# Kernel optimization log

Measured on AMD Instinct MI355X. Metric: run time of the kernel, lower is better.

Reference implementation:

```python
import jax, jax.numpy as jnp
import numpy as np

NINP = 850
NHID = 850
T = 128
B = 256
INITRANGE = 0.04
# DARTS published recurrent cell genotype
GENO_RECURRENT = [("sigmoid", 0), ("relu", 1), ("relu", 1), ("identity", 1),
                  ("tanh", 2), ("sigmoid", 5), ("tanh", 3), ("relu", 5)]
GENO_CONCAT = [1, 2, 3, 4, 5, 6, 7, 8]

ACT = {
    "tanh": jnp.tanh,
    "relu": jax.nn.relu,
    "sigmoid": jax.nn.sigmoid,
    "identity": lambda x: x,
}


def setup_inputs() -> dict:
    key = jax.random.key(0)
    ks = jax.random.split(key, 8)
    u = lambda k, s: jax.random.uniform(k, s, jnp.float32, -INITRANGE, INITRANGE)
    return {
        "inputs": jax.random.normal(ks[0], (T, B, NINP), jnp.float32),
        "hidden": jnp.zeros((1, B, NHID), jnp.float32),
        "W0_U": u(ks[1], (2 * NHID, 2 * NHID)),
        "W0_sigma": u(ks[2], (2 * NHID,)),
        "W0_V": u(ks[3], (2 * NHID, 2 * NHID)),
        "Ws_U": u(ks[4], (8, NHID, NHID)),
        "Ws_sigma": u(ks[5], (8, NHID)),
        "Ws_V": u(ks[6], (8, 2 * NHID, 2 * NHID)),
    }


def _lowrank_square(x, U, sig, V):
    # row == col: W = U @ diag(sig) @ V
    return ((x @ U) * sig) @ V


def _lowrank_wide(x, U, sig, V):
    # row < col (row=NHID, col=2*NHID): rectangular diag embeds rank=row into col dims
    t = (x @ U) * sig                               # [B, NHID]
    t = jnp.pad(t, ((0, 0), (0, V.shape[0] - t.shape[-1])))  # [B, 2*NHID]
    return t @ V                                    # [B, 2*NHID]


def _cell(x, h_prev, W0_U, W0_sigma, W0_V, Ws_U, Ws_sigma, Ws_V):
    xh = jnp.concatenate([x, h_prev], axis=-1)      # [B, 2*NHID]
    ch0 = _lowrank_square(xh, W0_U, W0_sigma, W0_V)  # [B, 2*NHID]
    c0 = jax.nn.sigmoid(ch0[:, :NHID])
    h0 = jnp.tanh(ch0[:, NHID:])
    s0 = h_prev + c0 * (h0 - h_prev)
    states = [s0]
    for i, (name, pred) in enumerate(GENO_RECURRENT):
        sp = states[pred]
        ch = _lowrank_wide(sp, Ws_U[i], Ws_sigma[i], Ws_V[i])
        c = jax.nn.sigmoid(ch[:, :NHID])
        hh = ACT[name](ch[:, NHID:])
        states.append(sp + c * (hh - sp))
    return jnp.mean(jnp.stack([states[i] for i in GENO_CONCAT], axis=-1), axis=-1)


def reference(inputs, hidden, W0_U, W0_sigma, W0_V, Ws_U, Ws_sigma, Ws_V):
    def step(h, x):
        h_new = _cell(x, h, W0_U, W0_sigma, W0_V, Ws_U, Ws_sigma, Ws_V)
        return h_new, h_new

    _, hiddens = jax.lax.scan(step, hidden[0], inputs)   # [T, B, NHID]
    return hiddens, hiddens[-1][None]
```

## Files before the change

### kernel.cpp

```cpp
#include <hip/hip_runtime.h>

typedef unsigned short u16;
typedef unsigned int u32;
typedef __attribute__((ext_vector_type(8))) short bf16x8;
typedef __attribute__((ext_vector_type(4))) float f32x4;

#define NHID 850
#define BATCH 256
#define TSTEPS 128
#define KPAD 896
#define KPAD0 1792
#define GRIDP 168

#define ACT_SIG 0
#define ACT_TANH 1
#define ACT_RELU 2
#define ACT_ID 3

__device__ __forceinline__ u16 f2bf(float f) {
  u32 u = __float_as_uint(f);
  u32 r = (u + 0x7fffu + ((u >> 16) & 1u)) >> 16;
  return (u16)r;
}
__device__ __forceinline__ float sigm(float x) { return 1.f / (1.f + __expf(-x)); }
__device__ __forceinline__ float act_apply(float x, int a) {
  if (a == ACT_SIG) return sigm(x);
  if (a == ACT_TANH) return 2.f * sigm(2.f * x) - 1.f;
  if (a == ACT_RELU) return fmaxf(x, 0.f);
  return x;
}

#define GLOAD_LDS16(gsrc, ldst)                                                     \
  __builtin_amdgcn_global_load_lds((const __attribute__((address_space(1))) void*)(gsrc), \
                                   (__attribute__((address_space(3))) void*)(ldst), 16, 0, 0)

__global__ void zero_kernel(uint4* p, u32 n) {
  u32 i = blockIdx.x * blockDim.x + threadIdx.x;
  const u32 stride = gridDim.x * blockDim.x;
  const uint4 z = {0u, 0u, 0u, 0u};
  for (; i < n; i += stride) p[i] = z;
}

__global__ void convert_kernel(const float* __restrict__ x, const float* __restrict__ h0,
                               u16* __restrict__ xb, u16* __restrict__ hb) {
  const u32 NX = (u32)TSTEPS * BATCH * NHID;
  u32 i = blockIdx.x * blockDim.x + threadIdx.x;
  if (i < NX) {
    const u32 tb = i / NHID, j = i - tb * NHID;
    xb[(size_t)tb * KPAD + j] = f2bf(x[i]);
  } else if (i < NX + (u32)BATCH * NHID) {
    const u32 k = i - NX;
    const u32 b = k / NHID, j = k - b * NHID;
    hb[(size_t)b * KPAD + j] = f2bf(h0[k]);
  }
}

__global__ __launch_bounds__(256) void prew0_kernel(const float* __restrict__ U,
                                                    const float* __restrict__ sig,
                                                    const float* __restrict__ V,
                                                    u16* __restrict__ outC,
                                                    u16* __restrict__ outH) {
  const int M = 1700, N = 1700, K = 1700;
  __shared__ float sA[64][17];
  __shared__ float sB[16][65];
  const int tid = threadIdx.x;
  const int tx = tid & 15, ty = tid >> 4;
  const int m0 = blockIdx.x * 64, n0 = blockIdx.y * 64;
  float acc[4][4] = {};
  for (int kb = 0; kb < K; kb += 16) {
#pragma unroll
    for (int i = 0; i < 4; ++i) {
      const int e = tid + i * 256;
      const int r = e >> 4, c = e & 15;
      const int mm = m0 + r, kk = kb + c;
      sA[r][c] = (mm < M && kk < K) ? U[(size_t)mm * K + kk] * sig[kk] : 0.f;
    }
#pragma unroll
    for (int i = 0; i < 4; ++i) {
      const int e = tid + i * 256;
      const int r = e >> 6, c = e & 63;
      const int kk = kb + r, nn = n0 + c;
      sB[r][c] = (kk < K && nn < N) ? V[(size_t)kk * N + nn] : 0.f;
    }
    __syncthreads();
#pragma unroll
    for (int k = 0; k < 16; ++k) {
      float a[4], b[4];
#pragma unroll
      for (int i = 0; i < 4; ++i) a[i] = sA[tx * 4 + i][k];
#pragma unroll
      for (int j = 0; j < 4; ++j) b[j] = sB[k][ty * 4 + j];
#pragma unroll
      for (int i = 0; i < 4; ++i)
#pragma unroll
        for (int j = 0; j < 4; ++j) acc[i][j] += a[i] * b[j];
    }
    __syncthreads();
  }
#pragma unroll
  for (int i = 0; i < 4; ++i) {
    const int m = m0 + tx * 4 + i;
    if (m >= M) continue;
    const int rp = (m < 850) ? m : m + 46;
#pragma unroll
    for (int j = 0; j < 4; ++j) {
      const int n = n0 + ty * 4 + j;
      if (n >= N) continue;
      if (n < 850) outC[(size_t)n * KPAD0 + rp] = f2bf(acc[i][j]);
      else outH[(size_t)(n - 850) * KPAD0 + rp] = f2bf(acc[i][j]);
    }
  }
}

__global__ __launch_bounds__(256) void prewn_kernel(const float* __restrict__ Uall,
                                                    const float* __restrict__ sigall,
                                                    const float* __restrict__ Vall,
                                                    u16* __restrict__ outBase) {
  const int M = 850, N = 1700, K = 850;
  const int ndi = blockIdx.z;
  const float* U = Uall + (size_t)ndi * 850 * 850;
  const float* sig = sigall + (size_t)ndi * 850;
  const float* V = Vall + (size_t)ndi * 1700 * 1700;
  u16* outC = outBase + (size_t)ndi * 2 * KPAD * KPAD;
  u16* outH = outC + (size_t)KPAD * KPAD;
  __shared__ float sA[64][17];
  __shared__ float sB[16][65];
  const int tid = threadIdx.x;
  const int tx = tid & 15, ty = tid >> 4;
  const int m0 = blockIdx.x * 64, n0 = blockIdx.y * 64;
  float acc[4][4] = {};
  for (int kb = 0; kb < K; kb += 16) {
#pragma unroll
    for (int i = 0; i < 4; ++i) {
      const int e = tid + i * 256;
      const int r = e >> 4, c = e & 15;
      const int mm = m0 + r, kk = kb + c;
      sA[r][c] = (mm < M && kk < K) ? U[(size_t)mm * K + kk] * sig[kk] : 0.f;
    }
#pragma unroll
    for (int i = 0; i < 4; ++i) {
      const int e = tid + i * 256;
      const int r = e >> 6, c = e & 63;
      const int kk = kb + r, nn = n0 + c;
      sB[r][c] = (kk < K && nn < N) ? V[(size_t)kk * 1700 + nn] : 0.f;
    }
    __syncthreads();
#pragma unroll
    for (int k = 0; k < 16; ++k) {
      float a[4], b[4];
#pragma unroll
      for (int i = 0; i < 4; ++i) a[i] = sA[tx * 4 + i][k];
#pragma unroll
      for (int j = 0; j < 4; ++j) b[j] = sB[k][ty * 4 + j];
#pragma unroll
      for (int i = 0; i < 4; ++i)
#pragma unroll
        for (int j = 0; j < 4; ++j) acc[i][j] += a[i] * b[j];
    }
    __syncthreads();
  }
#pragma unroll
  for (int i = 0; i < 4; ++i) {
    const int m = m0 + tx * 4 + i;
    if (m >= M) continue;
#pragma unroll
    for (int j = 0; j < 4; ++j) {
      const int n = n0 + ty * 4 + j;
      if (n >= N) continue;
      if (n < 850) outC[(size_t)n * KPAD + m] = f2bf(acc[i][j]);
      else outH[(size_t)(n - 850) * KPAD + m] = f2bf(acc[i][j]);
    }
  }
}

struct PArgs {
  const u16* xb;
  u16* hb;
  const u16* w0c; const u16* w0h;
  const u16* wnc[8]; const u16* wnh[8];
  const float* h0;
  float* out;
  float* sf[8];
  u16* sb[8];
  u32* bar;
};

__device__ __forceinline__ void grid_sync(u32* cnt, u32 target) {
  __syncthreads();
  if (threadIdx.x == 0) {
    __hip_atomic_fetch_add(cnt, 1u, __ATOMIC_RELEASE, __HIP_MEMORY_SCOPE_AGENT);
    while (__hip_atomic_load(cnt, __ATOMIC_RELAXED, __HIP_MEMORY_SCOPE_AGENT) < target)
      __builtin_amdgcn_s_sleep(8);
    __builtin_amdgcn_fence(__ATOMIC_ACQUIRE, "agent");
  }
  __syncthreads();
}

__device__ void gemm_stage(const u16* __restrict__ A, const u16* __restrict__ A2,
                           const u16* __restrict__ Bc, const u16* __restrict__ Bh,
                           const float* __restrict__ sp, float* __restrict__ outF,
                           u16* __restrict__ outB, int act, int Kt, int ktA, int bStride,
                           int m0, int n0, u16* lds) {
  const int tid = threadIdx.x;
  const int lane = tid & 63;
  const int w = tid >> 6;
  const int wm = (w & 1) * 32;
  const int wn = (w >> 1) * 32;
  f32x4 acc[2][2][2] = {};

  auto slot = [&](int buf, int s) { return lds + (size_t)(buf * 5 + s) * 4096; };
  auto stage = [&](int buf, int kt) {
    const u16* Asrc; int ktl;
    if (kt < ktA) { Asrc = A; ktl = kt; } else { Asrc = A2; ktl = kt - ktA; }
#pragma unroll
    for (int r2 = 0; r2 < 2; ++r2) {
      const int e = tid + 256 * r2;
      const int row = e >> 3;
      const int q = (e & 7) ^ (row & 7);
      GLOAD_LDS16(Asrc + (size_t)(m0 + row) * KPAD + ktl * 64 + q * 8, slot(buf, 0) + e * 8);
      GLOAD_LDS16(Bc + (size_t)(n0 + row) * bStride + kt * 64 + q * 8, slot(buf, 1) + e * 8);
      GLOAD_LDS16(Bh + (size_t)(n0 + row) * bStride + kt * 64 + q * 8, slot(buf, 2) + e * 8);
    }
  };

  stage(0, 0);
  int cur = 0;
  for (int kt = 0; kt < Kt; ++kt) {
    __syncthreads();
    if (kt + 1 < Kt) stage(cur ^ 1, kt + 1);
#pragma unroll
    for (int ks = 0; ks < 2; ++ks) {
      const int kg = lane >> 4;
      bf16x8 af[2], bc[2], bh[2];
#pragma unroll
      for (int mf = 0; mf < 2; ++mf) {
        const int row = wm + mf * 16 + (lane & 15);
        const int p = (ks * 4 + kg) ^ (row & 7);
        af[mf] = *(const bf16x8*)(slot(cur, 0) + row * 64 + p * 8);
      }
#pragma unroll
      for (int nf = 0; nf < 2; ++nf) {
        const int nr = wn + nf * 16 + (lane & 15);
        const int p = (ks * 4 + kg) ^ (nr & 7);
        bc[nf] = *(const bf16x8*)(slot(cur, 1) + nr * 64 + p * 8);
        bh[nf] = *(const bf16x8*)(slot(cur, 2) + nr * 64 + p * 8);
      }
#pragma unroll
      for (int mf = 0; mf < 2; ++mf)
#pragma unroll
        for (int nf = 0; nf < 2; ++nf) {
          acc[0][mf][nf] = __builtin_amdgcn_mfma_f32_16x16x32_bf16(af[mf], bc[nf], acc[0][mf][nf], 0, 0, 0);
          acc[1][mf][nf] = __builtin_amdgcn_mfma_f32_16x16x32_bf16(af[mf], bh[nf], acc[1][mf][nf], 0, 0, 0);
        }
    }
    cur ^= 1;
  }

  const int colb = n0 + wn + (lane & 15);
  const int rowb = m0 + wm + ((lane >> 4) << 2);
#pragma unroll
  for (int nf = 0; nf < 2; ++nf) {
    const int j = colb + nf * 16;
    if (j >= NHID) continue;
#pragma unroll
    for (int mf = 0; mf < 2; ++mf) {
      const int mb = rowb + mf * 16;
      const f32x4 ac = acc[0][mf][nf];
      const f32x4 ah = acc[1][mf][nf];
#pragma unroll
      for (int r = 0; r < 4; ++r) {
        const int m = mb + r;
        const float c = sigm(ac[r]);
        const float hv = act_apply(ah[r], act);
        const float spv = sp[m * NHID + j];
        const float s = spv + c * (hv - spv);
        outF[m * NHID + j] = s;
        outB[(size_t)m * KPAD + j] = f2bf(s);
      }
    }
  }
}

__device__ void final_tile(const PArgs& pa, int t, int m0, int n0, u16* lds) {
  const int tid = threadIdx.x;
  const int lane = tid & 63;
  const int w = tid >> 6;
  const int wm = (w & 1) * 32;
  const int wn = (w >> 1) * 32;
  const u16* A = pa.sb[5];
  const u16* Bp[4] = { pa.wnc[5], pa.wnh[5], pa.wnc[7], pa.wnh[7] };
  f32x4 acc[4][2][2] = {};

  auto slot = [&](int buf, int s) { return lds + (size_t)(buf * 5 + s) * 4096; };
  auto stage = [&](int buf, int kt) {
#pragma unroll
    for (int r2 = 0; r2 < 2; ++r2) {
      const int e = tid + 256 * r2;
      const int row = e >> 3;
      const int q = (e & 7) ^ (row & 7);
      GLOAD_LDS16(A + (size_t)(m0 + row) * KPAD + kt * 64 + q * 8, slot(buf, 0) + e * 8);
#pragma unroll
      for (int b = 0; b < 4; ++b)
        GLOAD_LDS16(Bp[b] + (size_t)(n0 + row) * KPAD + kt * 64 + q * 8, slot(buf, 1 + b) + e * 8);
    }
  };

  stage(0, 0);
  int cur = 0;
  for (int kt = 0; kt < 14; ++kt) {
    __syncthreads();
    if (kt + 1 < 14) stage(cur ^ 1, kt + 1);
#pragma unroll
    for (int ks = 0; ks < 2; ++ks) {
      const int kg = lane >> 4;
      bf16x8 af[2], bb[4][2];
#pragma unroll
      for (int mf = 0; mf < 2; ++mf) {
        const int row = wm + mf * 16 + (lane & 15);
        const int p = (ks * 4 + kg) ^ (row & 7);
        af[mf] = *(const bf16x8*)(slot(cur, 0) + row * 64 + p * 8);
      }
#pragma unroll
      for (int b = 0; b < 4; ++b)
#pragma unroll
        for (int nf = 0; nf < 2; ++nf) {
          const int nr = wn + nf * 16 + (lane & 15);
          const int p = (ks * 4 + kg) ^ (nr & 7);
          bb[b][nf] = *(const bf16x8*)(slot(cur, 1 + b) + nr * 64 + p * 8);
        }
#pragma unroll
      for (int b = 0; b < 4; ++b)
#pragma unroll
        for (int mf = 0; mf < 2; ++mf)
#pragma unroll
          for (int nf = 0; nf < 2; ++nf)
            acc[b][mf][nf] = __builtin_amdgcn_mfma_f32_16x16x32_bf16(af[mf], bb[b][nf], acc[b][mf][nf], 0, 0, 0);
    }
    cur ^= 1;
  }

  float* outH = pa.out + (size_t)t * BATCH * NHID;
  const int colb = n0 + wn + (lane & 15);
  const int rowb = m0 + wm + ((lane >> 4) << 2);
#pragma unroll
  for (int nf = 0; nf < 2; ++nf) {
    const int j = colb + nf * 16;
    if (j >= NHID) continue;
#pragma unroll
    for (int mf = 0; mf < 2; ++mf) {
      const int mb = rowb + mf * 16;
#pragma unroll
      for (int r = 0; r < 4; ++r) {
        const int m = mb + r;
        const int idx = m * NHID + j;
        const float s5v = pa.sf[5][idx];
        const float c6 = sigm(acc[0][mf][nf][r]);
        const float h6 = sigm(acc[1][mf][nf][r]);
        const float s6 = s5v + c6 * (h6 - s5v);
        const float c8 = sigm(acc[2][mf][nf][r]);
        const float h8 = fmaxf(acc[3][mf][nf][r], 0.f);
        const float s8 = s5v + c8 * (h8 - s5v);
        const float sum = pa.sf[1][idx] + pa.sf[2][idx] + pa.sf[3][idx] + pa.sf[4][idx]
                        + s5v + pa.sf[7][idx] + s6 + s8;
        const float h = sum * 0.125f;
        outH[idx] = h;
        pa.hb[(size_t)m * KPAD + j] = f2bf(h);
      }
    }
  }
}

__global__ __launch_bounds__(256) void cell_persist_kernel(PArgs pa) {
  __shared__ __align__(16) u16 lds[2 * 5 * 4096];
  const int bx = blockIdx.x;
  const u32 nb = gridDim.x;
  u32 gen = 0;

  for (int t = 0; t < TSTEPS; ++t) {
    const float* hprev = (t == 0) ? pa.h0 : (pa.out + (size_t)(t - 1) * BATCH * NHID);
    if (bx < 56) {
      const int m0 = (bx & 3) * 64, n0 = (bx >> 2) * 64;
      gemm_stage(pa.xb + (size_t)t * BATCH * KPAD, pa.hb, pa.w0c, pa.w0h,
                 hprev, pa.sf[0], pa.sb[0], ACT_TANH, 28, 14, KPAD0, m0, n0, lds);
    }
    grid_sync(pa.bar, ++gen * nb);
    if (bx < 56) {
      const int m0 = (bx & 3) * 64, n0 = (bx >> 2) * 64;
      gemm_stage(pa.sb[0], nullptr, pa.wnc[0], pa.wnh[0],
                 pa.sf[0], pa.sf[1], pa.sb[1], ACT_SIG, 14, 14, KPAD, m0, n0, lds);
    }
    grid_sync(pa.bar, ++gen * nb);
    if (bx < 168) {
      const int node = bx / 56, r = bx - node * 56;
      const int m0 = (r & 3) * 64, n0 = (r >> 2) * 64;
      const int act = (node == 2) ? ACT_ID : ACT_RELU;
      gemm_stage(pa.sb[1], nullptr, pa.wnc[1 + node], pa.wnh[1 + node],
                 pa.sf[1], pa.sf[2 + node], pa.sb[2 + node], act, 14, 14, KPAD, m0, n0, lds);
    }
    grid_sync(pa.bar, ++gen * nb);
    if (bx < 112) {
      const int g = bx / 56, r = bx - g * 56;
      const int m0 = (r & 3) * 64, n0 = (r >> 2) * 64;
      if (g == 0)
        gemm_stage(pa.sb[2], nullptr, pa.wnc[4], pa.wnh[4],
                   pa.sf[2], pa.sf[5], pa.sb[5], ACT_TANH, 14, 14, KPAD, m0, n0, lds);
      else
        gemm_stage(pa.sb[3], nullptr, pa.wnc[6], pa.wnh[6],
                   pa.sf[3], pa.sf[7], pa.sb[7], ACT_TANH, 14, 14, KPAD, m0, n0, lds);
    }
    grid_sync(pa.bar, ++gen * nb);
    if (bx < 56) {
      const int m0 = (bx & 3) * 64, n0 = (bx >> 2) * 64;
      final_tile(pa, t, m0, n0, lds);
    }
    grid_sync(pa.bar, ++gen * nb);
  }
}

extern "C" void kernel_launch(void* const* d_in, const int* in_sizes, int n_in,
                              void* d_out, int out_size, void* d_ws, size_t ws_size,
                              hipStream_t stream) {
  const float* x = (const float*)d_in[0];
  const float* h0 = (const float*)d_in[1];
  const float* W0U = (const float*)d_in[2];
  const float* W0s = (const float*)d_in[3];
  const float* W0V = (const float*)d_in[4];
  const float* WsU = (const float*)d_in[5];
  const float* Wss = (const float*)d_in[6];
  const float* WsV = (const float*)d_in[7];
  float* out = (float*)d_out;
  char* ws = (char*)d_ws;

  const size_t SZ_W0HALF = (size_t)KPAD * KPAD0 * 2;
  const size_t OFF_W0C = 0, OFF_W0H = SZ_W0HALF;
  const size_t OFF_WN = 2 * SZ_W0HALF;
  const size_t SZ_WNHALF = (size_t)KPAD * KPAD * 2;
  const size_t OFF_XB = OFF_WN + 16 * SZ_WNHALF;
  const size_t SZ_XB = (size_t)TSTEPS * BATCH * KPAD * 2;
  const size_t OFF_HB = OFF_XB + SZ_XB;
  const size_t SZ_HB = (size_t)BATCH * KPAD * 2;
  const size_t OFF_SF = OFF_HB + SZ_HB;
  const size_t SZ_SF = (size_t)BATCH * NHID * 4;
  const size_t OFF_SB = OFF_SF + 8 * SZ_SF;
  const size_t SZ_SB = (size_t)BATCH * KPAD * 2;
  const size_t OFF_BAR = OFF_SB + 8 * SZ_SB;
  const size_t TOTAL = OFF_BAR + 128;

  u16* w0c = (u16*)(ws + OFF_W0C);
  u16* w0h = (u16*)(ws + OFF_W0H);
  u16* wnBase = (u16*)(ws + OFF_WN);
  u16* xb = (u16*)(ws + OFF_XB);
  u16* hb = (u16*)(ws + OFF_HB);

  const size_t zbytes = (TOTAL <= ws_size) ? TOTAL : ws_size;
  zero_kernel<<<2048, 256, 0, stream>>>((uint4*)ws, (u32)((zbytes + 15) / 16));
  const u32 convTotal = (u32)TSTEPS * BATCH * NHID + (u32)BATCH * NHID;
  convert_kernel<<<(convTotal + 255) / 256, 256, 0, stream>>>(x, h0, xb, hb);
  prew0_kernel<<<dim3(27, 27), 256, 0, stream>>>(W0U, W0s, W0V, w0c, w0h);
  prewn_kernel<<<dim3(14, 27, 8), 256, 0, stream>>>(WsU, Wss, WsV, wnBase);

  PArgs pa;
  pa.xb = xb;
  pa.hb = hb;
  pa.w0c = w0c;
  pa.w0h = w0h;
  for (int i = 0; i < 8; ++i) {
    pa.wnc[i] = wnBase + (size_t)i * 2 * KPAD * KPAD;
    pa.wnh[i] = wnBase + (size_t)i * 2 * KPAD * KPAD + (size_t)KPAD * KPAD;
  }
  pa.h0 = h0;
  pa.out = out;
  for (int i = 0; i < 8; ++i) {
    pa.sf[i] = (float*)(ws + OFF_SF + (size_t)i * SZ_SF);
    pa.sb[i] = (u16*)(ws + OFF_SB + (size_t)i * SZ_SB);
  }
  pa.bar = (u32*)(ws + OFF_BAR);

  cell_persist_kernel<<<GRIDP, 256, 0, stream>>>(pa);

  hipMemcpyAsync(out + (size_t)TSTEPS * BATCH * NHID,
                 out + (size_t)(TSTEPS - 1) * BATCH * NHID,
                 (size_t)BATCH * NHID * sizeof(float), hipMemcpyDeviceToDevice, stream);
}
```

Measured before the change: 18.84 ms.

## Hoist input projection out of recurrence and keep weight slices resident in LDS

```diff
diff --git a/kernel.cpp b/kernel.cpp
--- a/kernel.cpp
+++ b/kernel.cpp
@@ -8,9 +8,8 @@
 #define NHID 850
 #define BATCH 256
 #define TSTEPS 128
-#define KPAD 896
-#define KPAD0 1792
-#define GRIDP 168
+#define KW 896
+#define GRIDP 243
 
 #define ACT_SIG 0
 #define ACT_TANH 1
@@ -22,6 +21,7 @@
   u32 r = (u + 0x7fffu + ((u >> 16) & 1u)) >> 16;
   return (u16)r;
 }
+__device__ __forceinline__ float bf2f(u16 v) { return __uint_as_float(((u32)v) << 16); }
 __device__ __forceinline__ float sigm(float x) { return 1.f / (1.f + __expf(-x)); }
 __device__ __forceinline__ float act_apply(float x, int a) {
   if (a == ACT_SIG) return sigm(x);
@@ -47,19 +47,31 @@
   u32 i = blockIdx.x * blockDim.x + threadIdx.x;
   if (i < NX) {
     const u32 tb = i / NHID, j = i - tb * NHID;
-    xb[(size_t)tb * KPAD + j] = f2bf(x[i]);
+    xb[(size_t)tb * KW + j] = f2bf(x[i]);
   } else if (i < NX + (u32)BATCH * NHID) {
     const u32 k = i - NX;
     const u32 b = k / NHID, j = k - b * NHID;
-    hb[(size_t)b * KPAD + j] = f2bf(h0[k]);
-  }
+    hb[(size_t)b * KW + j] = f2bf(h0[k]);
+  }
+}
+
+__device__ __forceinline__ int rmap64(int n) {
+  const int half = (n >= NHID) ? 1 : 0;
+  const int q = half ? (n - NHID) : n;
+  const int rem = q & 31;
+  return (q >> 5) * 64 + (((rem >> 4) << 1) | half) * 16 + (rem & 15);
+}
+__device__ __forceinline__ int rmap32(int n) {
+  const int half = (n >= NHID) ? 1 : 0;
+  const int q = half ? (n - NHID) : n;
+  return (q >> 4) * 32 + half * 16 + (q & 15);
 }
 
 __global__ __launch_bounds__(256) void prew0_kernel(const float* __restrict__ U,
                                                     const float* __restrict__ sig,
                                                     const float* __restrict__ V,
-                                                    u16* __restrict__ outC,
-                                                    u16* __restrict__ outH) {
+                                                    u16* __restrict__ w0x,
+                                                    u16* __restrict__ w0h) {
   const int M = 1700, N = 1700, K = 1700;
   __shared__ float sA[64][17];
   __shared__ float sB[16][65];
@@ -101,13 +113,13 @@
   for (int i = 0; i < 4; ++i) {
     const int m = m0 + tx * 4 + i;
     if (m >= M) continue;
-    const int rp = (m < 850) ? m : m + 46;
 #pragma unroll
     for (int j = 0; j < 4; ++j) {
       const int n = n0 + ty * 4 + j;
       if (n >= N) continue;
-      if (n < 850) outC[(size_t)n * KPAD0 + rp] = f2bf(acc[i][j]);
-      else outH[(size_t)(n - 850) * KPAD0 + rp] = f2bf(acc[i][j]);
+      const int r = rmap64(n);
+      if (m < NHID) w0x[(size_t)r * KW + m] = f2bf(acc[i][j]);
+      else w0h[(size_t)r * KW + (m - NHID)] = f2bf(acc[i][j]);
     }
   }
 }
@@ -121,8 +133,8 @@
   const float* U = Uall + (size_t)ndi * 850 * 850;
   const float* sig = sigall + (size_t)ndi * 850;
   const float* V = Vall + (size_t)ndi * 1700 * 1700;
-  u16* outC = outBase + (size_t)ndi * 2 * KPAD * KPAD;
-  u16* outH = outC + (size_t)KPAD * KPAD;
+  u16* wn = outBase + (size_t)ndi * 1728 * KW;
+  const bool dual = (ndi == 5 || ndi == 7);
   __shared__ float sA[64][17];
   __shared__ float sB[16][65];
   const int tid = threadIdx.x;
@@ -167,19 +179,96 @@
     for (int j = 0; j < 4; ++j) {
       const int n = n0 + ty * 4 + j;
       if (n >= N) continue;
-      if (n < 850) outC[(size_t)n * KPAD + m] = f2bf(acc[i][j]);
-      else outH[(size_t)(n - 850) * KPAD + m] = f2bf(acc[i][j]);
-    }
-  }
-}
-
-struct PArgs {
-  const u16* xb;
+      const int r = dual ? rmap32(n) : rmap64(n);
+      wn[(size_t)r * KW + m] = f2bf(acc[i][j]);
+    }
+  }
+}
+
+struct XArgs { const u16* A; const u16* B; u16* outU16; };
+
+__global__ __launch_bounds__(256) void xgemm_kernel(XArgs xa) {
+  __shared__ __align__(16) u16 lA[2][4096];
+  __shared__ __align__(16) u16 lB[2][4096];
+  const int tid = threadIdx.x;
+  const int lane = tid & 63;
+  const int w = tid >> 6;
+  const int wm = (w & 1) * 32;
+  const int wn = (w >> 1) * 32;
+  const int m0 = blockIdx.x * 64;
+  const int r0 = blockIdx.y * 64;
+  f32x4 acc[2][2] = {};
+
+  auto stage = [&](int buf, int kt) {
+#pragma unroll
+    for (int r2 = 0; r2 < 2; ++r2) {
+      const int e = tid + 256 * r2;
+      const int row = e >> 3;
+      const int q = (e & 7) ^ (row & 7);
+      GLOAD_LDS16(xa.A + (size_t)(m0 + row) * KW + kt * 64 + q * 8, &lA[buf][e * 8]);
+      GLOAD_LDS16(xa.B + (size_t)(r0 + row) * KW + kt * 64 + q * 8, &lB[buf][e * 8]);
+    }
+  };
+
+  stage(0, 0);
+  int cur = 0;
+  for (int kt = 0; kt < 14; ++kt) {
+    __syncthreads();
+    if (kt + 1 < 14) stage(cur ^ 1, kt + 1);
+#pragma unroll
+    for (int ks = 0; ks < 2; ++ks) {
+      const int kg = lane >> 4;
+      bf16x8 af[2], bb[2];
+#pragma unroll
+      for (int mf = 0; mf < 2; ++mf) {
+        const int row = wm + mf * 16 + (lane & 15);
+        const int p = (ks * 4 + kg) ^ (row & 7);
+        af[mf] = *(const bf16x8*)&lA[cur][row * 64 + p * 8];
+      }
+#pragma unroll
+      for (int nf = 0; nf < 2; ++nf) {
+        const int nr = wn + nf * 16 + (lane & 15);
+        const int p = (ks * 4 + kg) ^ (nr & 7);
+        bb[nf] = *(const bf16x8*)&lB[cur][nr * 64 + p * 8];
+      }
+#pragma unroll
+      for (int mf = 0; mf < 2; ++mf)
+#pragma unroll
+        for (int nf = 0; nf < 2; ++nf)
+          acc[mf][nf] = __builtin_amdgcn_mfma_f32_16x16x32_bf16(af[mf], bb[nf], acc[mf][nf], 0, 0, 0);
+    }
+    cur ^= 1;
+  }
+
+  const int u = lane & 15, rb = (lane >> 4) << 2;
+#pragma unroll
+  for (int nf = 0; nf < 2; ++nf) {
+    const int r = r0 + wn + nf * 16 + u;
+    const int jb = r >> 6, rem = r & 63, g = rem >> 4, uu = rem & 15;
+    const int half = g & 1;
+    const int j = jb * 32 + (g >> 1) * 16 + uu;
+    if (j >= NHID) continue;
+#pragma unroll
+    for (int mf = 0; mf < 2; ++mf) {
+#pragma unroll
+      for (int rr = 0; rr < 4; ++rr) {
+        const int m = m0 + wm + mf * 16 + rb + rr;
+        const int t = m >> 8, b = m & 255;
+        xa.outU16[(size_t)t * BATCH * 1700 + b * 1700 + half * NHID + j] =
+            f2bf(acc[mf][nf][rr]);
+      }
+    }
+  }
+}
+
+struct P2Args {
+  const u16* wfam[7];
+  const u16* w5;
+  const u16* w7;
   u16* hb;
-  const u16* w0c; const u16* w0h;
-  const u16* wnc[8]; const u16* wnh[8];
   const float* h0;
   float* out;
+  u16* outU16;
   float* sf[8];
   u16* sb[8];
   u32* bar;
@@ -196,222 +285,171 @@
   __syncthreads();
 }
 
-__device__ void gemm_stage(const u16* __restrict__ A, const u16* __restrict__ A2,
-                           const u16* __restrict__ Bc, const u16* __restrict__ Bh,
-                           const float* __restrict__ sp, float* __restrict__ outF,
-                           u16* __restrict__ outB, int act, int Kt, int ktA, int bStride,
-                           int m0, int n0, u16* lds) {
+__device__ __forceinline__ void job_mfma(const u16* __restrict__ A, const u16* wl,
+                                         f32x4 (&acc)[4][4]) {
+  const int lane = threadIdx.x & 63;
+  const int w = threadIdx.x >> 6;
+  const int kg = lane >> 4;
+  const int mbase = w * 64 + (lane & 15);
+  const u16* ar[4];
+#pragma unroll
+  for (int mf = 0; mf < 4; ++mf) ar[mf] = A + (size_t)(mbase + mf * 16) * KW + kg * 8;
+  bf16x8 a0[4], a1[4];
+#pragma unroll
+  for (int mf = 0; mf < 4; ++mf) a0[mf] = *(const bf16x8*)(ar[mf]);
+#pragma unroll 2
+  for (int s = 0; s < 28; ++s) {
+    if (s < 27) {
+#pragma unroll
+      for (int mf = 0; mf < 4; ++mf) a1[mf] = *(const bf16x8*)(ar[mf] + (s + 1) * 32);
+    }
+    bf16x8 bb[4];
+    const int kt = s >> 1, cb = (s & 1) * 4 + kg;
+#pragma unroll
+    for (int nf = 0; nf < 4; ++nf) {
+      const int rr = nf * 16 + (lane & 15);
+      bb[nf] = *(const bf16x8*)&wl[rr * KW + kt * 64 + ((cb ^ (rr & 7)) * 8)];
+    }
+#pragma unroll
+    for (int mf = 0; mf < 4; ++mf)
+#pragma unroll
+      for (int nf = 0; nf < 4; ++nf)
+        acc[mf][nf] = __builtin_amdgcn_mfma_f32_16x16x32_bf16(a0[mf], bb[nf], acc[mf][nf], 0, 0, 0);
+#pragma unroll
+    for (int mf = 0; mf < 4; ++mf) a0[mf] = a1[mf];
+  }
+}
+
+__device__ __forceinline__ void epi_std(const f32x4 (&acc)[4][4], int jb,
+                                        const float* __restrict__ sp,
+                                        float* __restrict__ outF, u16* __restrict__ outB,
+                                        int act) {
+  const int lane = threadIdx.x & 63, w = threadIdx.x >> 6;
+  const int u = lane & 15, rb = (lane >> 4) << 2;
+#pragma unroll
+  for (int p = 0; p < 2; ++p) {
+    const int j = jb * 32 + p * 16 + u;
+    if (j >= NHID) continue;
+#pragma unroll
+    for (int mf = 0; mf < 4; ++mf) {
+#pragma unroll
+      for (int r = 0; r < 4; ++r) {
+        const int m = w * 64 + mf * 16 + rb + r;
+        const float cv = sigm(acc[mf][2 * p][r]);
+        const float hv = act_apply(acc[mf][2 * p + 1][r], act);
+        const float spv = sp[m * NHID + j];
+        const float s = spv + cv * (hv - spv);
+        outF[m * NHID + j] = s;
+        outB[(size_t)m * KW + j] = f2bf(s);
+      }
+    }
+  }
+}
+
+__global__ __launch_bounds__(256) void cell_persist2(P2Args pa) {
+  __shared__ __align__(16) u16 wl[64 * KW];
+  const int bx = blockIdx.x;
   const int tid = threadIdx.x;
-  const int lane = tid & 63;
-  const int w = tid >> 6;
-  const int wm = (w & 1) * 32;
-  const int wn = (w >> 1) * 32;
-  f32x4 acc[2][2][2] = {};
-
-  auto slot = [&](int buf, int s) { return lds + (size_t)(buf * 5 + s) * 4096; };
-  auto stage = [&](int buf, int kt) {
-    const u16* Asrc; int ktl;
-    if (kt < ktA) { Asrc = A; ktl = kt; } else { Asrc = A2; ktl = kt - ktA; }
-#pragma unroll
-    for (int r2 = 0; r2 < 2; ++r2) {
-      const int e = tid + 256 * r2;
-      const int row = e >> 3;
-      const int q = (e & 7) ^ (row & 7);
-      GLOAD_LDS16(Asrc + (size_t)(m0 + row) * KPAD + ktl * 64 + q * 8, slot(buf, 0) + e * 8);
-      GLOAD_LDS16(Bc + (size_t)(n0 + row) * bStride + kt * 64 + q * 8, slot(buf, 1) + e * 8);
-      GLOAD_LDS16(Bh + (size_t)(n0 + row) * bStride + kt * 64 + q * 8, slot(buf, 2) + e * 8);
-    }
-  };
-
-  stage(0, 0);
-  int cur = 0;
-  for (int kt = 0; kt < Kt; ++kt) {
-    __syncthreads();
-    if (kt + 1 < Kt) stage(cur ^ 1, kt + 1);
-#pragma unroll
-    for (int ks = 0; ks < 2; ++ks) {
-      const int kg = lane >> 4;
-      bf16x8 af[2], bc[2], bh[2];
-#pragma unroll
-      for (int mf = 0; mf < 2; ++mf) {
-        const int row = wm + mf * 16 + (lane & 15);
-        const int p = (ks * 4 + kg) ^ (row & 7);
-        af[mf] = *(const bf16x8*)(slot(cur, 0) + row * 64 + p * 8);
+  int fam, jb;
+  if (bx < 189) { fam = bx / 27; jb = bx - fam * 27; }
+  else { fam = 7; jb = bx - 189; }
+
+  {
+    const u16* s0;
+    const u16* s1 = nullptr;
+    if (fam < 7) s0 = pa.wfam[fam] + (size_t)jb * 64 * KW;
+    else { s0 = pa.w5 + (size_t)jb * 32 * KW; s1 = pa.w7 + (size_t)jb * 32 * KW; }
+    for (int idx = tid; idx < 64 * (KW / 8); idx += 256) {
+      const int rr = idx / (KW / 8);
+      const int cc = idx - rr * (KW / 8);
+      const int kt = cc >> 3, c = cc & 7;
+      const u16* srow = (s1 && rr >= 32) ? s1 + (size_t)(rr - 32) * KW
+                                         : s0 + (size_t)rr * KW;
+      const uint4 v = *(const uint4*)(srow + cc * 8);
+      *(uint4*)&wl[rr * KW + kt * 64 + ((c ^ (rr & 7)) * 8)] = v;
+    }
+  }
+  __syncthreads();
+
+  u32 gen = 0;
+  const u32 nb = gridDim.x;
+  for (int t = 0; t < TSTEPS; ++t) {
+    if (fam == 0) {
+      const float* hprev = (t == 0) ? pa.h0 : pa.out + (size_t)(t - 1) * BATCH * NHID;
+      const u16* xw = pa.outU16 + (size_t)t * BATCH * 1700;
+      f32x4 acc[4][4] = {};
+      job_mfma(pa.hb, wl, acc);
+      const int lane = tid & 63, w = tid >> 6;
+      const int u = lane & 15, rb = (lane >> 4) << 2;
+#pragma unroll
+      for (int p = 0; p < 2; ++p) {
+        const int j = jb * 32 + p * 16 + u;
+        if (j >= NHID) continue;
+#pragma unroll
+        for (int mf = 0; mf < 4; ++mf) {
+#pragma unroll
+          for (int r = 0; r < 4; ++r) {
+            const int m = w * 64 + mf * 16 + rb + r;
+            const float xc = bf2f(xw[m * 1700 + j]);
+            const float xh = bf2f(xw[m * 1700 + NHID + j]);
+            const float cv = sigm(acc[mf][2 * p][r] + xc);
+            const float hv = act_apply(acc[mf][2 * p + 1][r] + xh, ACT_TANH);
+            const float spv = hprev[m * NHID + j];
+            const float s = spv + cv * (hv - spv);
+            pa.sf[0][m * NHID + j] = s;
+            pa.sb[0][(size_t)m * KW + j] = f2bf(s);
+          }
+        }
       }
-#pragma unroll
-      for (int nf = 0; nf < 2; ++nf) {
-        const int nr = wn + nf * 16 + (lane & 15);
-        const int p = (ks * 4 + kg) ^ (nr & 7);
-        bc[nf] = *(const bf16x8*)(slot(cur, 1) + nr * 64 + p * 8);
-        bh[nf] = *(const bf16x8*)(slot(cur, 2) + nr * 64 + p * 8);
+    }
+    grid_sync(pa.bar, ++gen * nb);
+    if (fam == 1) {
+      f32x4 acc[4][4] = {};
+      job_mfma(pa.sb[0], wl, acc);
+      epi_std(acc, jb, pa.sf[0], pa.sf[1], pa.sb[1], ACT_SIG);
+    }
+    grid_sync(pa.bar, ++gen * nb);
+    if (fam >= 2 && fam <= 4) {
+      f32x4 acc[4][4] = {};
+      job_mfma(pa.sb[1], wl, acc);
+      epi_std(acc, jb, pa.sf[1], pa.sf[fam], pa.sb[fam], (fam == 4) ? ACT_ID : ACT_RELU);
+    }
+    grid_sync(pa.bar, ++gen * nb);
+    if (fam == 5) {
+      f32x4 acc[4][4] = {};
+      job_mfma(pa.sb[2], wl, acc);
+      epi_std(acc, jb, pa.sf[2], pa.sf[5], pa.sb[5], ACT_TANH);
+    } else if (fam == 6) {
+      f32x4 acc[4][4] = {};
+      job_mfma(pa.sb[3], wl, acc);
+      epi_std(acc, jb, pa.sf[3], pa.sf[7], pa.sb[7], ACT_TANH);
+    }
+    grid_sync(pa.bar, ++gen * nb);
+    if (fam == 7) {
+      f32x4 acc[4][4] = {};
+      job_mfma(pa.sb[5], wl, acc);
+      float* outH = pa.out + (size_t)t * BATCH * NHID;
+      const int lane = tid & 63, w = tid >> 6;
+      const int u = lane & 15, rb = (lane >> 4) << 2;
+      const int j = jb * 16 + u;
+      if (j < NHID) {
+#pragma unroll
+        for (int mf = 0; mf < 4; ++mf) {
+#pragma unroll
+          for (int r = 0; r < 4; ++r) {
+            const int m = w * 64 + mf * 16 + rb + r;
+            const int idx = m * NHID + j;
+            const float s5v = pa.sf[5][idx];
+            const float s6 = s5v + sigm(acc[mf][0][r]) * (sigm(acc[mf][1][r]) - s5v);
+            const float s8 = s5v + sigm(acc[mf][2][r]) * (fmaxf(acc[mf][3][r], 0.f) - s5v);
+            const float sum = pa.sf[1][idx] + pa.sf[2][idx] + pa.sf[3][idx] + pa.sf[4][idx]
+                            + s5v + pa.sf[7][idx] + s6 + s8;
+            const float h = sum * 0.125f;
+            outH[idx] = h;
+            pa.hb[(size_t)m * KW + j] = f2bf(h);
+          }
+        }
       }
-#pragma unroll
-      for (int mf = 0; mf < 2; ++mf)
-#pragma unroll
-        for (int nf = 0; nf < 2; ++nf) {
-          acc[0][mf][nf] = __builtin_amdgcn_mfma_f32_16x16x32_bf16(af[mf], bc[nf], acc[0][mf][nf], 0, 0, 0);
-          acc[1][mf][nf] = __builtin_amdgcn_mfma_f32_16x16x32_bf16(af[mf], bh[nf], acc[1][mf][nf], 0, 0, 0);
-        }
-    }
-    cur ^= 1;
-  }
-
-  const int colb = n0 + wn + (lane & 15);
-  const int rowb = m0 + wm + ((lane >> 4) << 2);
-#pragma unroll
-  for (int nf = 0; nf < 2; ++nf) {
-    const int j = colb + nf * 16;
-    if (j >= NHID) continue;
-#pragma unroll
-    for (int mf = 0; mf < 2; ++mf) {
-      const int mb = rowb + mf * 16;
-      const f32x4 ac = acc[0][mf][nf];
-      const f32x4 ah = acc[1][mf][nf];
-#pragma unroll
-      for (int r = 0; r < 4; ++r) {
-        const int m = mb + r;
-        const float c = sigm(ac[r]);
-        const float hv = act_apply(ah[r], act);
-        const float spv = sp[m * NHID + j];
-        const float s = spv + c * (hv - spv);
-        outF[m * NHID + j] = s;
-        outB[(size_t)m * KPAD + j] = f2bf(s);
-      }
-    }
-  }
-}
-
-__device__ void final_tile(const PArgs& pa, int t, int m0, int n0, u16* lds) {
-  const int tid = threadIdx.x;
-  const int lane = tid & 63;
-  const int w = tid >> 6;
-  const int wm = (w & 1) * 32;
-  const int wn = (w >> 1) * 32;
-  const u16* A = pa.sb[5];
-  const u16* Bp[4] = { pa.wnc[5], pa.wnh[5], pa.wnc[7], pa.wnh[7] };
-  f32x4 acc[4][2][2] = {};
-
-  auto slot = [&](int buf, int s) { return lds + (size_t)(buf * 5 + s) * 4096; };
-  auto stage = [&](int buf, int kt) {
-#pragma unroll
-    for (int r2 = 0; r2 < 2; ++r2) {
-      const int e = tid + 256 * r2;
-      const int row = e >> 3;
-      const int q = (e & 7) ^ (row & 7);
-      GLOAD_LDS16(A + (size_t)(m0 + row) * KPAD + kt * 64 + q * 8, slot(buf, 0) + e * 8);
-#pragma unroll
-      for (int b = 0; b < 4; ++b)
-        GLOAD_LDS16(Bp[b] + (size_t)(n0 + row) * KPAD + kt * 64 + q * 8, slot(buf, 1 + b) + e * 8);
-    }
-  };
-
-  stage(0, 0);
-  int cur = 0;
-  for (int kt = 0; kt < 14; ++kt) {
-    __syncthreads();
-    if (kt + 1 < 14) stage(cur ^ 1, kt + 1);
-#pragma unroll
-    for (int ks = 0; ks < 2; ++ks) {
-      const int kg = lane >> 4;
-      bf16x8 af[2], bb[4][2];
-#pragma unroll
-      for (int mf = 0; mf < 2; ++mf) {
-        const int row = wm + mf * 16 + (lane & 15);
-        const int p = (ks * 4 + kg) ^ (row & 7);
-        af[mf] = *(const bf16x8*)(slot(cur, 0) + row * 64 + p * 8);
-      }
-#pragma unroll
-      for (int b = 0; b < 4; ++b)
-#pragma unroll
-        for (int nf = 0; nf < 2; ++nf) {
-          const int nr = wn + nf * 16 + (lane & 15);
-          const int p = (ks * 4 + kg) ^ (nr & 7);
-          bb[b][nf] = *(const bf16x8*)(slot(cur, 1 + b) + nr * 64 + p * 8);
-        }
-#pragma unroll
-      for (int b = 0; b < 4; ++b)
-#pragma unroll
-        for (int mf = 0; mf < 2; ++mf)
-#pragma unroll
-          for (int nf = 0; nf < 2; ++nf)
-            acc[b][mf][nf] = __builtin_amdgcn_mfma_f32_16x16x32_bf16(af[mf], bb[b][nf], acc[b][mf][nf], 0, 0, 0);
-    }
-    cur ^= 1;
-  }
-
-  float* outH = pa.out + (size_t)t * BATCH * NHID;
-  const int colb = n0 + wn + (lane & 15);
-  const int rowb = m0 + wm + ((lane >> 4) << 2);
-#pragma unroll
-  for (int nf = 0; nf < 2; ++nf) {
-    const int j = colb + nf * 16;
-    if (j >= NHID) continue;
-#pragma unroll
-    for (int mf = 0; mf < 2; ++mf) {
-      const int mb = rowb + mf * 16;
-#pragma unroll
-      for (int r = 0; r < 4; ++r) {
-        const int m = mb + r;
-        const int idx = m * NHID + j;
-        const float s5v = pa.sf[5][idx];
-        const float c6 = sigm(acc[0][mf][nf][r]);
-        const float h6 = sigm(acc[1][mf][nf][r]);
-        const float s6 = s5v + c6 * (h6 - s5v);
-        const float c8 = sigm(acc[2][mf][nf][r]);
-        const float h8 = fmaxf(acc[3][mf][nf][r], 0.f);
-        const float s8 = s5v + c8 * (h8 - s5v);
-        const float sum = pa.sf[1][idx] + pa.sf[2][idx] + pa.sf[3][idx] + pa.sf[4][idx]
-                        + s5v + pa.sf[7][idx] + s6 + s8;
-        const float h = sum * 0.125f;
-        outH[idx] = h;
-        pa.hb[(size_t)m * KPAD + j] = f2bf(h);
-      }
-    }
-  }
-}
-
-__global__ __launch_bounds__(256) void cell_persist_kernel(PArgs pa) {
-  __shared__ __align__(16) u16 lds[2 * 5 * 4096];
-  const int bx = blockIdx.x;
-  const u32 nb = gridDim.x;
-  u32 gen = 0;
-
-  for (int t = 0; t < TSTEPS; ++t) {
-    const float* hprev = (t == 0) ? pa.h0 : (pa.out + (size_t)(t - 1) * BATCH * NHID);
-    if (bx < 56) {
-      const int m0 = (bx & 3) * 64, n0 = (bx >> 2) * 64;
-      gemm_stage(pa.xb + (size_t)t * BATCH * KPAD, pa.hb, pa.w0c, pa.w0h,
-                 hprev, pa.sf[0], pa.sb[0], ACT_TANH, 28, 14, KPAD0, m0, n0, lds);
-    }
-    grid_sync(pa.bar, ++gen * nb);
-    if (bx < 56) {
-      const int m0 = (bx & 3) * 64, n0 = (bx >> 2) * 64;
-      gemm_stage(pa.sb[0], nullptr, pa.wnc[0], pa.wnh[0],
-                 pa.sf[0], pa.sf[1], pa.sb[1], ACT_SIG, 14, 14, KPAD, m0, n0, lds);
-    }
-    grid_sync(pa.bar, ++gen * nb);
-    if (bx < 168) {
-      const int node = bx / 56, r = bx - node * 56;
-      const int m0 = (r & 3) * 64, n0 = (r >> 2) * 64;
-      const int act = (node == 2) ? ACT_ID : ACT_RELU;
-      gemm_stage(pa.sb[1], nullptr, pa.wnc[1 + node], pa.wnh[1 + node],
-                 pa.sf[1], pa.sf[2 + node], pa.sb[2 + node], act, 14, 14, KPAD, m0, n0, lds);
-    }
-    grid_sync(pa.bar, ++gen * nb);
-    if (bx < 112) {
-      const int g = bx / 56, r = bx - g * 56;
-      const int m0 = (r & 3) * 64, n0 = (r >> 2) * 64;
-      if (g == 0)
-        gemm_stage(pa.sb[2], nullptr, pa.wnc[4], pa.wnh[4],
-                   pa.sf[2], pa.sf[5], pa.sb[5], ACT_TANH, 14, 14, KPAD, m0, n0, lds);
-      else
-        gemm_stage(pa.sb[3], nullptr, pa.wnc[6], pa.wnh[6],
-                   pa.sf[3], pa.sf[7], pa.sb[7], ACT_TANH, 14, 14, KPAD, m0, n0, lds);
-    }
-    grid_sync(pa.bar, ++gen * nb);
-    if (bx < 56) {
-      const int m0 = (bx & 3) * 64, n0 = (bx >> 2) * 64;
-      final_tile(pa, t, m0, n0, lds);
     }
     grid_sync(pa.bar, ++gen * nb);
   }
@@ -431,22 +469,22 @@
   float* out = (float*)d_out;
   char* ws = (char*)d_ws;
 
-  const size_t SZ_W0HALF = (size_t)KPAD * KPAD0 * 2;
-  const size_t OFF_W0C = 0, OFF_W0H = SZ_W0HALF;
-  const size_t OFF_WN = 2 * SZ_W0HALF;
-  const size_t SZ_WNHALF = (size_t)KPAD * KPAD * 2;
-  const size_t OFF_XB = OFF_WN + 16 * SZ_WNHALF;
-  const size_t SZ_XB = (size_t)TSTEPS * BATCH * KPAD * 2;
+  const size_t SZ_W = (size_t)1728 * KW * 2;
+  const size_t OFF_W0X = 0;
+  const size_t OFF_W0H = OFF_W0X + SZ_W;
+  const size_t OFF_WN = OFF_W0H + SZ_W;
+  const size_t OFF_XB = OFF_WN + 8 * SZ_W;
+  const size_t SZ_XB = (size_t)TSTEPS * BATCH * KW * 2;
   const size_t OFF_HB = OFF_XB + SZ_XB;
-  const size_t SZ_HB = (size_t)BATCH * KPAD * 2;
+  const size_t SZ_HB = (size_t)BATCH * KW * 2;
   const size_t OFF_SF = OFF_HB + SZ_HB;
   const size_t SZ_SF = (size_t)BATCH * NHID * 4;
   const size_t OFF_SB = OFF_SF + 8 * SZ_SF;
-  const size_t SZ_SB = (size_t)BATCH * KPAD * 2;
+  const size_t SZ_SB = (size_t)BATCH * KW * 2;
   const size_t OFF_BAR = OFF_SB + 8 * SZ_SB;
   const size_t TOTAL = OFF_BAR + 128;
 
-  u16* w0c = (u16*)(ws + OFF_W0C);
+  u16* w0x = (u16*)(ws + OFF_W0X);
   u16* w0h = (u16*)(ws + OFF_W0H);
   u16* wnBase = (u16*)(ws + OFF_WN);
   u16* xb = (u16*)(ws + OFF_XB);
@@ -456,27 +494,32 @@
   zero_kernel<<<2048, 256, 0, stream>>>((uint4*)ws, (u32)((zbytes + 15) / 16));
   const u32 convTotal = (u32)TSTEPS * BATCH * NHID + (u32)BATCH * NHID;
   convert_kernel<<<(convTotal + 255) / 256, 256, 0, stream>>>(x, h0, xb, hb);
-  prew0_kernel<<<dim3(27, 27), 256, 0, stream>>>(W0U, W0s, W0V, w0c, w0h);
+  prew0_kernel<<<dim3(27, 27), 256, 0, stream>>>(W0U, W0s, W0V, w0x, w0h);
   prewn_kernel<<<dim3(14, 27, 8), 256, 0, stream>>>(WsU, Wss, WsV, wnBase);
 
-  PArgs pa;
-  pa.xb = xb;
+  XArgs xa;
+  xa.A = xb;
+  xa.B = w0x;
+  xa.outU16 = (u16*)d_out;
+  xgemm_kernel<<<dim3(TSTEPS * BATCH / 64, 27), 256, 0, stream>>>(xa);
+
+  auto wn = [&](int i) { return wnBase + (size_t)i * 1728 * KW; };
+  P2Args pa;
+  pa.wfam[0] = w0h;
+  pa.wfam[1] = wn(0); pa.wfam[2] = wn(1); pa.wfam[3] = wn(2); pa.wfam[4] = wn(3);
+  pa.wfam[5] = wn(4); pa.wfam[6] = wn(6);
+  pa.w5 = wn(5); pa.w7 = wn(7);
   pa.hb = hb;
-  pa.w0c = w0c;
-  pa.w0h = w0h;
-  for (int i = 0; i < 8; ++i) {
-    pa.wnc[i] = wnBase + (size_t)i * 2 * KPAD * KPAD;
-    pa.wnh[i] = wnBase + (size_t)i * 2 * KPAD * KPAD + (size_t)KPAD * KPAD;
-  }
   pa.h0 = h0;
   pa.out = out;
+  pa.outU16 = (u16*)d_out;
   for (int i = 0; i < 8; ++i) {
     pa.sf[i] = (float*)(ws + OFF_SF + (size_t)i * SZ_SF);
     pa.sb[i] = (u16*)(ws + OFF_SB + (size_t)i * SZ_SB);
   }
   pa.bar = (u32*)(ws + OFF_BAR);
 
-  cell_persist_kernel<<<GRIDP, 256, 0, stream>>>(pa);
+  cell_persist2<<<GRIDP, 256, 0, stream>>>(pa);
 
   hipMemcpyAsync(out + (size_t)TSTEPS * BATCH * NHID,
                  out + (size_t)(TSTEPS - 1) * BATCH * NHID,
```

Measured after the change: 36.98 ms. 96.3% more time.
